# Kernel tuning notes

Hardware: AMD Instinct MI355X
Metric: run time of the kernel (lower is better)

The kernel has to match this reference:

```python
import jax, jax.numpy as jnp
import numpy as np
import math

B, L, DIM = 2, 2048, 1024
HEADS = 16
DH = DIM // HEADS  # 64
M_IALSH = 2
U_IALSH = 0.75
NEG = -1e4  # additive mask value for non-matching hash buckets


def setup_inputs() -> dict:
    key = jax.random.key(0)
    k0, k1, k2, k3 = jax.random.split(key, 4)
    return {
        "hidden_states": jax.random.normal(k0, (B, L, DIM), jnp.float32),
        "qk_w": jax.random.normal(k1, (DIM, DIM), jnp.float32) * 0.02,
        "qk_b": jnp.zeros((DIM,), jnp.float32),
        "v_w": jax.random.normal(k2, (DIM, DIM), jnp.float32) * 0.02,
        "v_b": jnp.zeros((DIM,), jnp.float32),
        "hash_a": jax.random.normal(k3, (DH + M_IALSH,), jnp.float32),
    }


def _ialsh_mask(qkh, hash_a):
    # qkh: (b, h, l, dh). IALSH (Improved Asymmetric LSH for MIPS):
    # keys scaled so max norm per (b,h) is U; P(x)=[x, 1/2-||x||^2, 1/2-||x||^4]
    # queries unit-normalized;        Q(x)=[x/||x||, 0, 0]
    norms = jnp.linalg.norm(qkh, axis=-1, keepdims=True)          # (b,h,l,1)
    max_norm = jnp.max(norms, axis=2, keepdims=True)              # (b,h,1,1)
    xk = qkh * (U_IALSH / jnp.maximum(max_norm, 1e-12))
    nk2 = jnp.sum(xk * xk, axis=-1, keepdims=True)                # ||x||^2
    P = jnp.concatenate([xk, 0.5 - nk2, 0.5 - nk2 * nk2], axis=-1)
    q_unit = qkh / jnp.maximum(norms, 1e-12)
    zeros = jnp.zeros_like(nk2)
    Q = jnp.concatenate([q_unit, zeros, zeros], axis=-1)
    hq = (Q @ hash_a) >= 0.0                                      # (b,h,l) sign hash
    hk = (P @ hash_a) >= 0.0
    same = hq[..., :, None] == hk[..., None, :]                   # (b,h,l,l)
    return jnp.where(same, 0.0, NEG).astype(qkh.dtype)


def reference(hidden_states, qk_w, qk_b, v_w, v_b, hash_a):
    b, l, d = hidden_states.shape
    qk = hidden_states @ qk_w.T + qk_b                            # shared Q/K projection
    v = hidden_states @ v_w.T + v_b

    def split(x):  # (b,l,d) -> (b,h,l,dh)
        return x.reshape(b, l, HEADS, DH).transpose(0, 2, 1, 3)

    qkh, vh = split(qk), split(v)
    scores = jnp.einsum('bhqd,bhkd->bhqk', qkh, qkh) / math.sqrt(DH)
    scores = scores + _ialsh_mask(qkh, hash_a)
    probs = jax.nn.softmax(scores, axis=-1)  # dropout = identity (eval mode)
    ctx = jnp.einsum('bhqk,bhkd->bhqd', probs, vh)
    return ctx.transpose(0, 2, 1, 3).reshape(b, l, d)
```

## Files before the change

kernel.cpp:

```cpp
#include <hip/hip_runtime.h>

typedef unsigned short u16;
typedef unsigned char  u8;
typedef unsigned int   u32;

typedef short bf16x8 __attribute__((ext_vector_type(8)));
typedef float f32x4  __attribute__((ext_vector_type(4)));

#define DEV __device__ __forceinline__

#if __has_builtin(__builtin_amdgcn_exp2f)
#define EXP2(x) __builtin_amdgcn_exp2f(x)
#else
#define EXP2(x) exp2f(x)
#endif

DEV u16 f2bf(float x) {
  u32 u = __builtin_bit_cast(u32, x);
  u32 r = (u + 0x7fffu + ((u >> 16) & 1u)) >> 16;
  return (u16)r;
}
DEV float bf2f(u16 h) {
  u32 u = ((u32)h) << 16;
  return __builtin_bit_cast(float, u);
}
DEV f32x4 mfma16(bf16x8 a, bf16x8 b, f32x4 c) {
  return __builtin_amdgcn_mfma_f32_16x16x32_bf16(a, b, c, 0, 0, 0);
}

__global__ __launch_bounds__(256) void split_kernel(
    const float* __restrict__ x, u16* __restrict__ hi, u16* __restrict__ lo, int n) {
  int i = blockIdx.x * 256 + threadIdx.x;
  if (i >= n) return;
  float v = x[i];
  u16 h = f2bf(v);
  hi[i] = h;
  lo[i] = f2bf(v - bf2f(h));
}

__global__ __launch_bounds__(256) void ca_kernel(
    const float* __restrict__ W, const float* __restrict__ ha, double* __restrict__ ca) {
  int idx = blockIdx.x * 256 + threadIdx.x;
  int h = idx >> 10, k = idx & 1023;
  double s = 0.0;
#pragma unroll 8
  for (int j = 0; j < 64; ++j)
    s += (double)W[(size_t)(h * 64 + j) * 1024 + k] * (double)ha[j];
  ca[idx] = s;
}

__global__ __launch_bounds__(256) void d_kernel(
    const float* __restrict__ hid, const double* __restrict__ ca, float* __restrict__ dq) {
  const int row  = blockIdx.x * 4 + (threadIdx.x >> 6);
  const int lane = threadIdx.x & 63;
  const int b = row >> 11, l = row & 2047;
  double acc[16];
#pragma unroll
  for (int h = 0; h < 16; ++h) acc[h] = 0.0;
  const float* hp = hid + (size_t)row * 1024;
  for (int k = lane; k < 1024; k += 64) {
    const double hv = (double)hp[k];
#pragma unroll
    for (int h = 0; h < 16; ++h) acc[h] += hv * ca[h * 1024 + k];
  }
#pragma unroll
  for (int h = 0; h < 16; ++h) {
    double v = acc[h];
#pragma unroll
    for (int off = 32; off; off >>= 1) v += __shfl_xor(v, off, 64);
    if (lane == 0) dq[(size_t)(b * 16 + h) * 2048 + l] = (float)v;
  }
}

__global__ __launch_bounds__(256) void gemm_fused(
    const u16* __restrict__ hHi, const u16* __restrict__ hLo,
    const u16* __restrict__ wqHi, const u16* __restrict__ wqLo,
    const u16* __restrict__ wvHi,
    const float* __restrict__ qk_b, const float* __restrict__ v_b,
    u16* __restrict__ qkB, u16* __restrict__ vT, float* __restrict__ n2A) {
  constexpr int K = 1024;
  __shared__ u16 Ah[128 * 32];
  __shared__ u16 Bh[128 * 32];
  __shared__ u16 Al[128 * 32];
  __shared__ u16 Bl[128 * 32];

  const int zsel = blockIdx.z;
  const int m0 = (zsel ? blockIdx.y : blockIdx.x) * 128;
  const int n0 = (zsel ? blockIdx.x : blockIdx.y) * 128;
  const int CN = zsel ? 4096 : 1024;
  const u16* __restrict__ Ahi = zsel ? wvHi : hHi;
  const u16* __restrict__ Bhi = zsel ? hHi : wqHi;
  u16* __restrict__ Cb = zsel ? vT : qkB;
  const int terms = zsel ? 1 : 3;

  const int tid = threadIdx.x;
  const int wave = tid >> 6, lane = tid & 63;
  const int quad = lane >> 4, lm = lane & 15;
  const int wr = wave >> 1, wc = wave & 1;

  f32x4 acc[4][4];
#pragma unroll
  for (int i = 0; i < 4; ++i)
#pragma unroll
    for (int j = 0; j < 4; ++j) acc[i][j] = {0.f, 0.f, 0.f, 0.f};

  for (int k0 = 0; k0 < K; k0 += 32) {
    __syncthreads();
#pragma unroll
    for (int it = 0; it < 2; ++it) {
      const int rb = wave * 2 + it;
      const int row = rb * 16 + (lane >> 2);
      const int ch = lane & 3;
      const size_t goffA = (size_t)(m0 + row) * K + k0 + ch * 8;
      const size_t goffB = (size_t)(n0 + row) * K + k0 + ch * 8;
      __builtin_amdgcn_global_load_lds(
          (const __attribute__((address_space(1))) void*)(Ahi + goffA),
          (__attribute__((address_space(3))) void*)(Ah + rb * 512), 16, 0, 0);
      __builtin_amdgcn_global_load_lds(
          (const __attribute__((address_space(1))) void*)(Bhi + goffB),
          (__attribute__((address_space(3))) void*)(Bh + rb * 512), 16, 0, 0);
      if (terms > 1) {
        __builtin_amdgcn_global_load_lds(
            (const __attribute__((address_space(1))) void*)(hLo + goffA),
            (__attribute__((address_space(3))) void*)(Al + rb * 512), 16, 0, 0);
        __builtin_amdgcn_global_load_lds(
            (const __attribute__((address_space(1))) void*)(wqLo + goffB),
            (__attribute__((address_space(3))) void*)(Bl + rb * 512), 16, 0, 0);
      }
    }
    __syncthreads();

    bf16x8 a_h[4], b_h[4], a_l[4], b_l[4];
#pragma unroll
    for (int i = 0; i < 4; ++i)
      a_h[i] = *(const bf16x8*)(Ah + (wr * 64 + i * 16 + lm) * 32 + quad * 8);
#pragma unroll
    for (int j = 0; j < 4; ++j)
      b_h[j] = *(const bf16x8*)(Bh + (wc * 64 + j * 16 + lm) * 32 + quad * 8);
    if (terms > 1) {
#pragma unroll
      for (int i = 0; i < 4; ++i)
        a_l[i] = *(const bf16x8*)(Al + (wr * 64 + i * 16 + lm) * 32 + quad * 8);
#pragma unroll
      for (int j = 0; j < 4; ++j)
        b_l[j] = *(const bf16x8*)(Bl + (wc * 64 + j * 16 + lm) * 32 + quad * 8);
#pragma unroll
      for (int i = 0; i < 4; ++i)
#pragma unroll
        for (int j = 0; j < 4; ++j) {
          acc[i][j] = mfma16(a_h[i], b_h[j], acc[i][j]);
          acc[i][j] = mfma16(a_h[i], b_l[j], acc[i][j]);
          acc[i][j] = mfma16(a_l[i], b_h[j], acc[i][j]);
        }
    } else {
#pragma unroll
      for (int i = 0; i < 4; ++i)
#pragma unroll
        for (int j = 0; j < 4; ++j)
          acc[i][j] = mfma16(a_h[i], b_h[j], acc[i][j]);
    }
  }

  if (zsel == 0) {
    const int hidx = blockIdx.y * 2 + wc;
#pragma unroll
    for (int i = 0; i < 4; ++i) {
      float nn[4] = {0.f, 0.f, 0.f, 0.f};
#pragma unroll
      for (int j = 0; j < 4; ++j) {
        const int col = n0 + wc * 64 + j * 16 + lm;
        const float bv = qk_b[col];
#pragma unroll
        for (int r = 0; r < 4; ++r) {
          const int row = m0 + wr * 64 + i * 16 + quad * 4 + r;
          const float val = acc[i][j][r] + bv;
          Cb[(size_t)row * CN + col] = f2bf(val);
          nn[r] += val * val;
        }
      }
#pragma unroll
      for (int r = 0; r < 4; ++r)
#pragma unroll
        for (int off = 1; off < 16; off <<= 1) nn[r] += __shfl_xor(nn[r], off, 64);
      if (lm == 0) {
        const int row = m0 + wr * 64 + i * 16 + quad * 4;
        const int b = row >> 11, l = row & 2047;
        *(float4*)&n2A[(size_t)(b * 16 + hidx) * 2048 + l] =
            make_float4(nn[0], nn[1], nn[2], nn[3]);
      }
    }
  } else {
#pragma unroll
    for (int i = 0; i < 4; ++i)
#pragma unroll
      for (int r = 0; r < 4; ++r) {
        const int row = m0 + wr * 64 + i * 16 + quad * 4 + r;
        const float bv = v_b[row];
#pragma unroll
        for (int j = 0; j < 4; ++j) {
          const int col = n0 + wc * 64 + j * 16 + lm;
          Cb[(size_t)row * CN + col] = f2bf(acc[i][j][r] + bv);
        }
      }
  }
}

__global__ __launch_bounds__(256) void bits_kernel(
    const float* __restrict__ n2A, const float* __restrict__ dq,
    const float* __restrict__ ha, u8* __restrict__ hqA, u8* __restrict__ hkA) {
  const int bh = blockIdx.x;
  const int tid = threadIdx.x;
  const int wave = tid >> 6, lane = tid & 63;
  __shared__ float red[4];
  const float* n2p = n2A + (size_t)bh * 2048;
  float4 v0 = ((const float4*)n2p)[tid];
  float4 v1 = ((const float4*)n2p)[tid + 256];
  float lmax = fmaxf(fmaxf(fmaxf(v0.x, v0.y), fmaxf(v0.z, v0.w)),
                     fmaxf(fmaxf(v1.x, v1.y), fmaxf(v1.z, v1.w)));
#pragma unroll
  for (int off = 1; off < 64; off <<= 1) lmax = fmaxf(lmax, __shfl_xor(lmax, off, 64));
  if (lane == 0) red[wave] = lmax;
  __syncthreads();
  const float maxn2 = fmaxf(fmaxf(red[0], red[1]), fmaxf(red[2], red[3]));
  const float s = 0.75f / fmaxf(sqrtf(maxn2), 1e-12f);
  const float a64 = ha[64], a65 = ha[65];
#pragma unroll
  for (int it = 0; it < 8; ++it) {
    const int l = it * 256 + tid;
    const float dv = dq[(size_t)bh * 2048 + l];
    const float n2 = n2p[l];
    const float nk2 = s * s * n2;
    const float hkdot = s * dv + (0.5f - nk2) * a64 + (0.5f - nk2 * nk2) * a65;
    hqA[(size_t)bh * 2048 + l] = (dv >= 0.f) ? 1 : 0;
    hkA[(size_t)bh * 2048 + l] = (hkdot >= 0.f) ? 1 : 0;
  }
}

__global__ __launch_bounds__(256, 4) void attn_kernel(
    const u16* __restrict__ qkb, const u16* __restrict__ vT,
    const u8* __restrict__ hqA, const u8* __restrict__ hkA, float* __restrict__ out) {
  __shared__ u16 Ks[2][4096];
  __shared__ u16 Vs[2][4096];
  __shared__ u16 Ps[4][1024];

  const int qt = blockIdx.x;
  const int bh = blockIdx.y;
  const int b = bh >> 4, h = bh & 15;
  const int tid = threadIdx.x, wave = tid >> 6, lane = tid & 63;
  const int quad = lane >> 4, lm = lane & 15;
  const int lx = lm & 7;
  const int r8 = lane >> 3, ch = lane & 7;
  const int q0 = qt * 64;

  const u16* qbase = qkb + (size_t)b * 2048 * 1024 + h * 64;
  const u16* vtb = vT + (size_t)h * 64 * 4096 + b * 2048;
  const u8* hkp = hkA + (size_t)bh * 2048;

  bf16x8 aQ[2];
#pragma unroll
  for (int c = 0; c < 2; ++c)
    aQ[c] = *(const bf16x8*)(qbase +
        (size_t)(q0 + wave * 16 + lm) * 1024 + c * 32 + quad * 8);
  u8 hqb[4];
  {
    const u8* hqp = hqA + (size_t)bh * 2048 + q0 + wave * 16;
#pragma unroll
    for (int r = 0; r < 4; ++r) hqb[r] = hqp[quad * 4 + r];
  }

  const int srow = wave * 16;
  auto stage = [&](int kt, int buf) {
#pragma unroll
    for (int i = 0; i < 2; ++i) {
      const int row = srow + i * 8 + r8;
      const int sw = (ch ^ (row & 7)) * 8;
      __builtin_amdgcn_global_load_lds(
          (const __attribute__((address_space(1))) void*)(
              qbase + (size_t)(kt * 64 + row) * 1024 + sw),
          (__attribute__((address_space(3))) void*)(&Ks[buf][(srow + i * 8) * 64]),
          16, 0, 0);
      __builtin_amdgcn_global_load_lds(
          (const __attribute__((address_space(1))) void*)(
              vtb + (size_t)row * 4096 + kt * 64 + sw),
          (__attribute__((address_space(3))) void*)(&Vs[buf][(srow + i * 8) * 64]),
          16, 0, 0);
    }
  };

  stage(0, 0);

  f32x4 acc_o[4], accL;
  accL = {0.f, 0.f, 0.f, 0.f};
#pragma unroll
  for (int j = 0; j < 4; ++j) acc_o[j] = {0.f, 0.f, 0.f, 0.f};
  const bf16x8 ones = {0x3F80, 0x3F80, 0x3F80, 0x3F80, 0x3F80, 0x3F80, 0x3F80, 0x3F80};
  const float SCL = 0.18033688f;
  const float M0 = -4.3280854f;
  const float M1 = -1.4430768e4f;

  __syncthreads();

  for (int kt = 0; kt < 32; ++kt) {
    const int cur = kt & 1;
    if (kt < 31) stage(kt + 1, cur ^ 1);

    u8 hkv[4];
#pragma unroll
    for (int nb = 0; nb < 4; ++nb) hkv[nb] = hkp[kt * 64 + nb * 16 + lm];

    f32x4 cs[4];
#pragma unroll
    for (int nb = 0; nb < 4; ++nb) cs[nb] = {0.f, 0.f, 0.f, 0.f};
#pragma unroll
    for (int c = 0; c < 2; ++c)
#pragma unroll
      for (int nb = 0; nb < 4; ++nb) {
        bf16x8 bK = *(const bf16x8*)&Ks[cur][(nb * 16 + lm) * 64 + (((c * 4 + quad) ^ lx) * 8)];
        cs[nb] = mfma16(aQ[c], bK, cs[nb]);
      }

#pragma unroll
    for (int nb = 0; nb < 4; ++nb)
#pragma unroll
      for (int r = 0; r < 4; ++r) {
        const float msel = (hqb[r] == hkv[nb]) ? M0 : M1;
        const float p = EXP2(__builtin_fmaf(cs[nb][r], SCL, msel));
        const int prow = quad * 4 + r;
        const int pc = (nb * 2 + (lm >> 3)) ^ (prow & 7);
        union { float f; u16 hw[2]; } u;
        u.f = p;
        Ps[wave][prow * 64 + pc * 8 + lx] = u.hw[1];
      }

    bf16x8 aP[2];
#pragma unroll
    for (int c = 0; c < 2; ++c) {
      aP[c] = *(const bf16x8*)&Ps[wave][lm * 64 + (((c * 4 + quad) ^ lx) * 8)];
      accL = mfma16(aP[c], ones, accL);
    }
#pragma unroll
    for (int c = 0; c < 2; ++c)
#pragma unroll
      for (int j = 0; j < 4; ++j) {
        bf16x8 bV = *(const bf16x8*)&Vs[cur][(j * 16 + lm) * 64 + (((c * 4 + quad) ^ lx) * 8)];
        acc_o[j] = mfma16(aP[c], bV, acc_o[j]);
      }

    __syncthreads();
  }

#pragma unroll
  for (int r = 0; r < 4; ++r) {
    const float inv = 1.0f / accL[r];
    float* op = out + (size_t)(b * 2048 + q0 + wave * 16 + quad * 4 + r) * 1024 + h * 64;
#pragma unroll
    for (int j = 0; j < 4; ++j) op[j * 16 + lm] = acc_o[j][r] * inv;
  }
}

extern "C" void kernel_launch(void* const* d_in, const int* in_sizes, int n_in,
                              void* d_out, int out_size, void* d_ws, size_t ws_size,
                              hipStream_t stream) {
  const float* hidden = (const float*)d_in[0];
  const float* qk_w   = (const float*)d_in[1];
  const float* qk_b   = (const float*)d_in[2];
  const float* v_w    = (const float*)d_in[3];
  const float* v_b    = (const float*)d_in[4];
  const float* hash_a = (const float*)d_in[5];
  float* out = (float*)d_out;

  char* base = (char*)d_ws;
  size_t off = 0;
  auto take = [&](size_t bytes) -> char* {
    char* r = base + off;
    off += (bytes + 255) & ~(size_t)255;
    return r;
  };
  const size_t NH = 4194304;
  const size_t NW = 1048576;
  u16* hHi  = (u16*)take(NH * 2);
  u16* hLo  = (u16*)take(NH * 2);
  u16* wqHi = (u16*)take(NW * 2);
  u16* wqLo = (u16*)take(NW * 2);
  u16* wvHi = (u16*)take(NW * 2);
  u16* wvLo = (u16*)take(NW * 2);
  u16* qkB  = (u16*)take(NH * 2);
  u16* vT   = (u16*)take(NH * 2);
  double* ca = (double*)take(16 * 1024 * 8);
  float* dq  = (float*)take(65536 * 4);
  float* n2A = (float*)take(65536 * 4);
  u8* hqA = (u8*)take(65536);
  u8* hkA = (u8*)take(65536);

  hipLaunchKernelGGL(split_kernel, dim3(NH / 256), dim3(256), 0, stream, hidden, hHi, hLo, (int)NH);
  hipLaunchKernelGGL(split_kernel, dim3(NW / 256), dim3(256), 0, stream, qk_w, wqHi, wqLo, (int)NW);
  hipLaunchKernelGGL(split_kernel, dim3(NW / 256), dim3(256), 0, stream, v_w, wvHi, wvLo, (int)NW);
  hipLaunchKernelGGL(ca_kernel, dim3(64), dim3(256), 0, stream, qk_w, hash_a, ca);
  hipLaunchKernelGGL(d_kernel, dim3(1024), dim3(256), 0, stream, hidden, ca, dq);
  hipLaunchKernelGGL(gemm_fused, dim3(32, 8, 2), dim3(256), 0, stream,
                     hHi, hLo, wqHi, wqLo, wvHi, qk_b, v_b, qkB, vT, n2A);
  hipLaunchKernelGGL(bits_kernel, dim3(32), dim3(256), 0, stream, n2A, dq, hash_a, hqA, hkA);
  hipLaunchKernelGGL(attn_kernel, dim3(32, 32), dim3(256), 0, stream, qkB, vT, hqA, hkA, out);
}
```

Baseline: 245.8 us.

## Fuse QK and V projections into one double-buffered GEMM sharing hidden tiles

Merges the three split launches into one kernel and stops producing the unused low part of the V weights. The QK and V projection GEMMs are restructured into a single kernel with 64x128 tiles. Each hidden-state tile is loaded once and feeds both the 3-term QK product and the V^T product, with double-buffered LDS staging and a launch-bounds occupancy hint. This cuts the redundant hidden-state reads and the loop's synchronisation stalls, at the cost of more LDS per block (64 KB), more registers, and transposed vT stores.

```diff
diff --git a/kernel.cpp b/kernel.cpp
--- a/kernel.cpp
+++ b/kernel.cpp
@@ -28,14 +28,33 @@
   return __builtin_amdgcn_mfma_f32_16x16x32_bf16(a, b, c, 0, 0, 0);
 }
 
-__global__ __launch_bounds__(256) void split_kernel(
-    const float* __restrict__ x, u16* __restrict__ hi, u16* __restrict__ lo, int n) {
+#define GLDS(gptr, lptr)                                                  \
+  __builtin_amdgcn_global_load_lds(                                       \
+      (const __attribute__((address_space(1))) void*)(gptr),              \
+      (__attribute__((address_space(3))) void*)(lptr), 16, 0, 0)
+
+__global__ __launch_bounds__(256) void split3_kernel(
+    const float* __restrict__ hid, const float* __restrict__ wq,
+    const float* __restrict__ wv,
+    u16* __restrict__ hHi, u16* __restrict__ hLo,
+    u16* __restrict__ wqHi, u16* __restrict__ wqLo, u16* __restrict__ wvHi) {
+  const int NH = 4194304, NW = 1048576;
   int i = blockIdx.x * 256 + threadIdx.x;
-  if (i >= n) return;
-  float v = x[i];
-  u16 h = f2bf(v);
-  hi[i] = h;
-  lo[i] = f2bf(v - bf2f(h));
+  if (i < NH) {
+    float v = hid[i];
+    u16 t = f2bf(v);
+    hHi[i] = t;
+    hLo[i] = f2bf(v - bf2f(t));
+  } else if (i < NH + NW) {
+    int j = i - NH;
+    float v = wq[j];
+    u16 t = f2bf(v);
+    wqHi[j] = t;
+    wqLo[j] = f2bf(v - bf2f(t));
+  } else {
+    int j = i - NH - NW;
+    wvHi[j] = f2bf(wv[j]);
+  }
 }
 
 __global__ __launch_bounds__(256) void ca_kernel(
@@ -72,137 +91,120 @@
   }
 }
 
-__global__ __launch_bounds__(256) void gemm_fused(
+__global__ __launch_bounds__(256, 2) void gemm_fused(
     const u16* __restrict__ hHi, const u16* __restrict__ hLo,
     const u16* __restrict__ wqHi, const u16* __restrict__ wqLo,
     const u16* __restrict__ wvHi,
     const float* __restrict__ qk_b, const float* __restrict__ v_b,
     u16* __restrict__ qkB, u16* __restrict__ vT, float* __restrict__ n2A) {
   constexpr int K = 1024;
-  __shared__ u16 Ah[128 * 32];
-  __shared__ u16 Bh[128 * 32];
-  __shared__ u16 Al[128 * 32];
-  __shared__ u16 Bl[128 * 32];
-
-  const int zsel = blockIdx.z;
-  const int m0 = (zsel ? blockIdx.y : blockIdx.x) * 128;
-  const int n0 = (zsel ? blockIdx.x : blockIdx.y) * 128;
-  const int CN = zsel ? 4096 : 1024;
-  const u16* __restrict__ Ahi = zsel ? wvHi : hHi;
-  const u16* __restrict__ Bhi = zsel ? hHi : wqHi;
-  u16* __restrict__ Cb = zsel ? vT : qkB;
-  const int terms = zsel ? 1 : 3;
-
-  const int tid = threadIdx.x;
-  const int wave = tid >> 6, lane = tid & 63;
+  __shared__ u16 S[2][16384];
+  const int tid = threadIdx.x, wave = tid >> 6, lane = tid & 63;
   const int quad = lane >> 4, lm = lane & 15;
   const int wr = wave >> 1, wc = wave & 1;
-
-  f32x4 acc[4][4];
-#pragma unroll
-  for (int i = 0; i < 4; ++i)
-#pragma unroll
-    for (int j = 0; j < 4; ++j) acc[i][j] = {0.f, 0.f, 0.f, 0.f};
-
-  for (int k0 = 0; k0 < K; k0 += 32) {
-    __syncthreads();
+  const int m0 = blockIdx.x * 64, n0 = blockIdx.y * 128;
+  const int ch = lane & 3, rA = lane >> 2;
+
+  auto stage = [&](int kt, int buf) {
+    const int k0 = kt * 32;
+    const int rowA = wave * 16 + rA;
+    GLDS(hHi + (size_t)(m0 + rowA) * K + k0 + ch * 8, &S[buf][0 + wave * 512]);
+    GLDS(hLo + (size_t)(m0 + rowA) * K + k0 + ch * 8, &S[buf][2048 + wave * 512]);
 #pragma unroll
     for (int it = 0; it < 2; ++it) {
       const int rb = wave * 2 + it;
-      const int row = rb * 16 + (lane >> 2);
-      const int ch = lane & 3;
-      const size_t goffA = (size_t)(m0 + row) * K + k0 + ch * 8;
-      const size_t goffB = (size_t)(n0 + row) * K + k0 + ch * 8;
-      __builtin_amdgcn_global_load_lds(
-          (const __attribute__((address_space(1))) void*)(Ahi + goffA),
-          (__attribute__((address_space(3))) void*)(Ah + rb * 512), 16, 0, 0);
-      __builtin_amdgcn_global_load_lds(
-          (const __attribute__((address_space(1))) void*)(Bhi + goffB),
-          (__attribute__((address_space(3))) void*)(Bh + rb * 512), 16, 0, 0);
-      if (terms > 1) {
-        __builtin_amdgcn_global_load_lds(
-            (const __attribute__((address_space(1))) void*)(hLo + goffA),
-            (__attribute__((address_space(3))) void*)(Al + rb * 512), 16, 0, 0);
-        __builtin_amdgcn_global_load_lds(
-            (const __attribute__((address_space(1))) void*)(wqLo + goffB),
-            (__attribute__((address_space(3))) void*)(Bl + rb * 512), 16, 0, 0);
-      }
-    }
+      const int row = rb * 16 + rA;
+      GLDS(wqHi + (size_t)(n0 + row) * K + k0 + ch * 8, &S[buf][4096 + rb * 512]);
+      GLDS(wqLo + (size_t)(n0 + row) * K + k0 + ch * 8, &S[buf][8192 + rb * 512]);
+      GLDS(wvHi + (size_t)(n0 + row) * K + k0 + ch * 8, &S[buf][12288 + rb * 512]);
+    }
+  };
+
+  f32x4 aq[2][4], av[4][2];
+#pragma unroll
+  for (int i = 0; i < 2; ++i)
+#pragma unroll
+    for (int j = 0; j < 4; ++j) aq[i][j] = {0.f, 0.f, 0.f, 0.f};
+#pragma unroll
+  for (int i = 0; i < 4; ++i)
+#pragma unroll
+    for (int j = 0; j < 2; ++j) av[i][j] = {0.f, 0.f, 0.f, 0.f};
+
+  stage(0, 0);
+  __syncthreads();
+
+  for (int kt = 0; kt < 32; ++kt) {
+    const int cur = kt & 1;
+    if (kt < 31) stage(kt + 1, cur ^ 1);
+
+    bf16x8 a_h[2], a_l[2], b_h[4], b_l[4], w_h[4];
+#pragma unroll
+    for (int i = 0; i < 2; ++i) {
+      a_h[i] = *(const bf16x8*)&S[cur][(wr * 32 + i * 16 + lm) * 32 + quad * 8];
+      a_l[i] = *(const bf16x8*)&S[cur][2048 + (wr * 32 + i * 16 + lm) * 32 + quad * 8];
+    }
+#pragma unroll
+    for (int j = 0; j < 4; ++j) {
+      b_h[j] = *(const bf16x8*)&S[cur][4096 + (wc * 64 + j * 16 + lm) * 32 + quad * 8];
+      b_l[j] = *(const bf16x8*)&S[cur][8192 + (wc * 64 + j * 16 + lm) * 32 + quad * 8];
+      w_h[j] = *(const bf16x8*)&S[cur][12288 + (wc * 64 + j * 16 + lm) * 32 + quad * 8];
+    }
+#pragma unroll
+    for (int i = 0; i < 2; ++i)
+#pragma unroll
+      for (int j = 0; j < 4; ++j) {
+        aq[i][j] = mfma16(a_h[i], b_h[j], aq[i][j]);
+        aq[i][j] = mfma16(a_h[i], b_l[j], aq[i][j]);
+        aq[i][j] = mfma16(a_l[i], b_h[j], aq[i][j]);
+      }
+#pragma unroll
+    for (int iv = 0; iv < 4; ++iv)
+#pragma unroll
+      for (int jv = 0; jv < 2; ++jv)
+        av[iv][jv] = mfma16(w_h[iv], a_h[jv], av[iv][jv]);
+
     __syncthreads();
-
-    bf16x8 a_h[4], b_h[4], a_l[4], b_l[4];
-#pragma unroll
-    for (int i = 0; i < 4; ++i)
-      a_h[i] = *(const bf16x8*)(Ah + (wr * 64 + i * 16 + lm) * 32 + quad * 8);
-#pragma unroll
-    for (int j = 0; j < 4; ++j)
-      b_h[j] = *(const bf16x8*)(Bh + (wc * 64 + j * 16 + lm) * 32 + quad * 8);
-    if (terms > 1) {
-#pragma unroll
-      for (int i = 0; i < 4; ++i)
-        a_l[i] = *(const bf16x8*)(Al + (wr * 64 + i * 16 + lm) * 32 + quad * 8);
-#pragma unroll
-      for (int j = 0; j < 4; ++j)
-        b_l[j] = *(const bf16x8*)(Bl + (wc * 64 + j * 16 + lm) * 32 + quad * 8);
-#pragma unroll
-      for (int i = 0; i < 4; ++i)
-#pragma unroll
-        for (int j = 0; j < 4; ++j) {
-          acc[i][j] = mfma16(a_h[i], b_h[j], acc[i][j]);
-          acc[i][j] = mfma16(a_h[i], b_l[j], acc[i][j]);
-          acc[i][j] = mfma16(a_l[i], b_h[j], acc[i][j]);
-        }
-    } else {
-#pragma unroll
-      for (int i = 0; i < 4; ++i)
-#pragma unroll
-        for (int j = 0; j < 4; ++j)
-          acc[i][j] = mfma16(a_h[i], b_h[j], acc[i][j]);
-    }
-  }
-
-  if (zsel == 0) {
-    const int hidx = blockIdx.y * 2 + wc;
-#pragma unroll
-    for (int i = 0; i < 4; ++i) {
-      float nn[4] = {0.f, 0.f, 0.f, 0.f};
-#pragma unroll
-      for (int j = 0; j < 4; ++j) {
-        const int col = n0 + wc * 64 + j * 16 + lm;
-        const float bv = qk_b[col];
-#pragma unroll
-        for (int r = 0; r < 4; ++r) {
-          const int row = m0 + wr * 64 + i * 16 + quad * 4 + r;
-          const float val = acc[i][j][r] + bv;
-          Cb[(size_t)row * CN + col] = f2bf(val);
-          nn[r] += val * val;
-        }
-      }
-#pragma unroll
-      for (int r = 0; r < 4; ++r)
-#pragma unroll
-        for (int off = 1; off < 16; off <<= 1) nn[r] += __shfl_xor(nn[r], off, 64);
-      if (lm == 0) {
-        const int row = m0 + wr * 64 + i * 16 + quad * 4;
-        const int b = row >> 11, l = row & 2047;
-        *(float4*)&n2A[(size_t)(b * 16 + hidx) * 2048 + l] =
-            make_float4(nn[0], nn[1], nn[2], nn[3]);
-      }
-    }
-  } else {
-#pragma unroll
-    for (int i = 0; i < 4; ++i)
+  }
+
+  const int hidx = blockIdx.y * 2 + wc;
+#pragma unroll
+  for (int i = 0; i < 2; ++i) {
+    float nn[4] = {0.f, 0.f, 0.f, 0.f};
+#pragma unroll
+    for (int j = 0; j < 4; ++j) {
+      const int col = n0 + wc * 64 + j * 16 + lm;
+      const float bv = qk_b[col];
 #pragma unroll
       for (int r = 0; r < 4; ++r) {
-        const int row = m0 + wr * 64 + i * 16 + quad * 4 + r;
-        const float bv = v_b[row];
-#pragma unroll
-        for (int j = 0; j < 4; ++j) {
-          const int col = n0 + wc * 64 + j * 16 + lm;
-          Cb[(size_t)row * CN + col] = f2bf(acc[i][j][r] + bv);
-        }
-      }
-  }
+        const int row = m0 + wr * 32 + i * 16 + quad * 4 + r;
+        const float val = aq[i][j][r] + bv;
+        qkB[(size_t)row * 1024 + col] = f2bf(val);
+        nn[r] += val * val;
+      }
+    }
+#pragma unroll
+    for (int r = 0; r < 4; ++r)
+#pragma unroll
+      for (int off = 1; off < 16; off <<= 1) nn[r] += __shfl_xor(nn[r], off, 64);
+    if (lm == 0) {
+      const int row = m0 + wr * 32 + i * 16 + quad * 4;
+      const int b = row >> 11, l = row & 2047;
+      *(float4*)&n2A[(size_t)(b * 16 + hidx) * 2048 + l] =
+          make_float4(nn[0], nn[1], nn[2], nn[3]);
+    }
+  }
+#pragma unroll
+  for (int iv = 0; iv < 4; ++iv)
+#pragma unroll
+    for (int r = 0; r < 4; ++r) {
+      const int vcol = n0 + wc * 64 + iv * 16 + quad * 4 + r;
+      const float bv = v_b[vcol];
+#pragma unroll
+      for (int jv = 0; jv < 2; ++jv) {
+        const int tok = m0 + wr * 32 + jv * 16 + lm;
+        vT[(size_t)vcol * 4096 + tok] = f2bf(av[iv][jv][r] + bv);
+      }
+    }
 }
 
 __global__ __launch_bounds__(256) void bits_kernel(
@@ -274,16 +276,8 @@
     for (int i = 0; i < 2; ++i) {
       const int row = srow + i * 8 + r8;
       const int sw = (ch ^ (row & 7)) * 8;
-      __builtin_amdgcn_global_load_lds(
-          (const __attribute__((address_space(1))) void*)(
-              qbase + (size_t)(kt * 64 + row) * 1024 + sw),
-          (__attribute__((address_space(3))) void*)(&Ks[buf][(srow + i * 8) * 64]),
-          16, 0, 0);
-      __builtin_amdgcn_global_load_lds(
-          (const __attribute__((address_space(1))) void*)(
-              vtb + (size_t)row * 4096 + kt * 64 + sw),
-          (__attribute__((address_space(3))) void*)(&Vs[buf][(srow + i * 8) * 64]),
-          16, 0, 0);
+      GLDS(qbase + (size_t)(kt * 64 + row) * 1024 + sw, &Ks[buf][(srow + i * 8) * 64]);
+      GLDS(vtb + (size_t)row * 4096 + kt * 64 + sw, &Vs[buf][(srow + i * 8) * 64]);
     }
   };
 
@@ -383,7 +377,6 @@
   u16* wqHi = (u16*)take(NW * 2);
   u16* wqLo = (u16*)take(NW * 2);
   u16* wvHi = (u16*)take(NW * 2);
-  u16* wvLo = (u16*)take(NW * 2);
   u16* qkB  = (u16*)take(NH * 2);
   u16* vT   = (u16*)take(NH * 2);
   double* ca = (double*)take(16 * 1024 * 8);
@@ -392,12 +385,11 @@
   u8* hqA = (u8*)take(65536);
   u8* hkA = (u8*)take(65536);
 
-  hipLaunchKernelGGL(split_kernel, dim3(NH / 256), dim3(256), 0, stream, hidden, hHi, hLo, (int)NH);
-  hipLaunchKernelGGL(split_kernel, dim3(NW / 256), dim3(256), 0, stream, qk_w, wqHi, wqLo, (int)NW);
-  hipLaunchKernelGGL(split_kernel, dim3(NW / 256), dim3(256), 0, stream, v_w, wvHi, wvLo, (int)NW);
+  hipLaunchKernelGGL(split3_kernel, dim3((NH + 2 * NW) / 256), dim3(256), 0, stream,
+                     hidden, qk_w, v_w, hHi, hLo, wqHi, wqLo, wvHi);
   hipLaunchKernelGGL(ca_kernel, dim3(64), dim3(256), 0, stream, qk_w, hash_a, ca);
   hipLaunchKernelGGL(d_kernel, dim3(1024), dim3(256), 0, stream, hidden, ca, dq);
-  hipLaunchKernelGGL(gemm_fused, dim3(32, 8, 2), dim3(256), 0, stream,
+  hipLaunchKernelGGL(gemm_fused, dim3(64, 8), dim3(256), 0, stream,
                      hHi, hLo, wqHi, wqLo, wvHi, qk_b, v_b, qkB, vT, n2A);
   hipLaunchKernelGGL(bits_kernel, dim3(32), dim3(256), 0, stream, n2A, dq, hash_a, hqA, hkA);
   hipLaunchKernelGGL(attn_kernel, dim3(32, 32), dim3(256), 0, stream, qkB, vT, hqA, hkA, out);
```

After: 229.9 us. 1.07x faster.
